# Performance work log

Measured on AMD Instinct MI355X. Metric: run time of the kernel, lower is better.

## Reference

```python
import jax, jax.numpy as jnp
import numpy as np

B, N, E, H, DEPTH = 2, 2048, 1024, 8, 12
D = E // H // 2  # head_dim = 64
LN_EPS = 1e-5


def setup_inputs() -> dict:
    key = jax.random.key(0)
    ks = jax.random.split(key, 10)
    w = lambda k: jax.random.normal(k, (E, E), jnp.float32) * (E ** -0.5)
    lp = lambda k: jax.random.normal(k, (D,), jnp.float32) * 0.1
    return {
        "x": jax.random.normal(ks[0], (B, N, E), jnp.float32),
        "Wq": w(ks[1]), "Wk": w(ks[2]), "Wv": w(ks[3]), "Wo": w(ks[4]),
        "lq1": lp(ks[5]), "lk1": lp(ks[6]), "lq2": lp(ks[7]), "lk2": lp(ks[8]),
        "ln_g": jnp.ones((2 * D,), jnp.float32),
        "ln_b": jnp.zeros((2 * D,), jnp.float32),
    }


def reference(x, Wq, Wk, Wv, Wo, lq1, lk1, lq2, lk2, ln_g, ln_b):
    b, n, e = x.shape
    lam_init = 0.8 - 0.6 * np.exp(-0.3 * DEPTH)  # lambda_init_fn(depth)
    # projections; split into 2H half-heads of dim D for q,k; H heads of dim 2D for v
    q = (x @ Wq).reshape(b, n, 2 * H, D).transpose(0, 2, 1, 3) * (D ** -0.5)  # [b,2H,n,D]
    k = (x @ Wk).reshape(b, n, 2 * H, D).transpose(0, 2, 1, 3)                # [b,2H,n,D]
    v = (x @ Wv).reshape(b, n, H, 2 * D).transpose(0, 2, 1, 3)                # [b,H,n,2D]
    scores = jnp.einsum('bhqd,bhkd->bhqk', q, k)                              # [b,2H,n,n]
    attn = jax.nn.softmax(scores, axis=-1).reshape(b, H, 2, n, n)
    lam = jnp.exp(jnp.sum(lq1 * lk1)) - jnp.exp(jnp.sum(lq2 * lk2)) + lam_init
    w_diff = attn[:, :, 0] - lam * attn[:, :, 1]                              # [b,H,n,n]
    o = jnp.einsum('bhqk,bhkd->bhqd', w_diff, v)                              # [b,H,n,2D]
    # per-head LayerNorm over channel dim 2D
    mu = o.mean(-1, keepdims=True)
    var = ((o - mu) ** 2).mean(-1, keepdims=True)
    o = (o - mu) * jax.lax.rsqrt(var + LN_EPS) * ln_g + ln_b
    o = o.transpose(0, 2, 1, 3).reshape(b, n, e)
    return o @ Wo
```

## Files before the change

kernel.cpp:

```cpp
#include <hip/hip_runtime.h>
#include <hip/hip_bf16.h>
#include <math.h>

#define B_ 2
#define N_ 2048
#define E_ 1024
#define H_ 8

typedef __attribute__((ext_vector_type(8))) short frag8;
typedef __attribute__((ext_vector_type(4))) float f32x4;
typedef __attribute__((ext_vector_type(16))) float f32x16;
typedef __attribute__((ext_vector_type(8))) unsigned short u16x8;

constexpr float LAM_INIT = 0.7836057665316245f;
constexpr float LOG2E = 1.4426950408889634f;
constexpr float EXP2_GUARD = -23.083120654f;

static __device__ __forceinline__ float fast_exp2(float x) {
#if __has_builtin(__builtin_amdgcn_exp2f)
  return __builtin_amdgcn_exp2f(x);
#else
  return exp2f(x);
#endif
}

static __device__ __forceinline__ ushort f2bf(float f) {
  union { float f; unsigned u; } v; v.f = f;
  unsigned r = (v.u + 0x7FFFu + ((v.u >> 16) & 1u)) >> 16;
  return (ushort)r;
}

static __device__ __forceinline__ unsigned pkbf(float a, float b) {
  __hip_bfloat162 h = __float22bfloat162_rn(make_float2(a, b));
  return *(unsigned*)&h;
}

static __device__ __forceinline__ float bf2f_lo(unsigned u) {
  union { unsigned u; float f; } v; v.u = u << 16; return v.f;
}
static __device__ __forceinline__ float bf2f_hi(unsigned u) {
  union { unsigned u; float f; } v; v.u = u & 0xFFFF0000u; return v.f;
}

static __device__ __forceinline__ void async16(const void* g, void* l) {
  __builtin_amdgcn_global_load_lds((const __attribute__((address_space(1))) void*)g,
                                   (__attribute__((address_space(3))) void*)l, 16, 0, 0);
}

static __device__ __forceinline__ frag8 mkfrag(unsigned p0, unsigned p1,
                                               unsigned p2, unsigned p3) {
  auto r02 = __builtin_amdgcn_permlane32_swap((int)p0, (int)p2, false, false);
  auto r13 = __builtin_amdgcn_permlane32_swap((int)p1, (int)p3, false, false);
  union { unsigned u[4]; frag8 f; } u;
  u.u[0] = (unsigned)r02[0];
  u.u[1] = (unsigned)r13[0];
  u.u[2] = (unsigned)r02[1];
  u.u[3] = (unsigned)r13[1];
  return u.f;
}

__global__ __launch_bounds__(256) void prep_kernel(
    const float* __restrict__ x,
    const float* __restrict__ Wq, const float* __restrict__ Wk,
    const float* __restrict__ Wv, const float* __restrict__ Wo,
    const float* __restrict__ lq1, const float* __restrict__ lk1,
    const float* __restrict__ lq2, const float* __restrict__ lk2,
    ushort* __restrict__ xb, ushort* __restrict__ wqkvt, ushort* __restrict__ wot,
    float* __restrict__ lam_out) {
  __shared__ ushort t[64][72];
  const int bx = blockIdx.x;
  const int tid = threadIdx.x;
  if (bx < 2048) {
    int i = bx * 256 + tid;
    const float4* sp = (const float4*)x + (size_t)i * 2;
    float4 a = sp[0], b = sp[1];
    u16x8 o;
    o[0] = f2bf(a.x); o[1] = f2bf(a.y); o[2] = f2bf(a.z); o[3] = f2bf(a.w);
    o[4] = f2bf(b.x); o[5] = f2bf(b.y); o[6] = f2bf(b.z); o[7] = f2bf(b.w);
    *(u16x8*)(xb + (size_t)i * 8) = o;
  } else if (bx < 3072) {
    int idx = bx - 2048;
    int sel = idx >> 8, rem = idx & 255;
    const float* W = (sel == 0) ? Wq : (sel == 1) ? Wk : (sel == 2) ? Wv : Wo;
    ushort* Wt = (sel < 3) ? (wqkvt + (size_t)sel * 1048576) : wot;
    const int c0 = (rem & 15) * 64, r0 = (rem >> 4) * 64;
    {
      int r = tid >> 2, cc = (tid & 3) * 16;
      const float* sp = W + (size_t)(r0 + r) * 1024 + c0 + cc;
      #pragma unroll
      for (int j = 0; j < 4; j++) {
        float4 a = *(const float4*)(sp + j * 4);
        t[cc + j * 4 + 0][r] = f2bf(a.x);
        t[cc + j * 4 + 1][r] = f2bf(a.y);
        t[cc + j * 4 + 2][r] = f2bf(a.z);
        t[cc + j * 4 + 3][r] = f2bf(a.w);
      }
    }
    __syncthreads();
    int c = tid >> 2, rr = (tid & 3) * 16;
    ushort* dp = Wt + (size_t)(c0 + c) * 1024 + r0 + rr;
    *(u16x8*)dp = *(u16x8*)&t[c][rr];
    *(u16x8*)(dp + 8) = *(u16x8*)&t[c][rr + 8];
  } else {
    if (tid < 64) {
      float t1 = lq1[tid] * lk1[tid];
      float t2 = lq2[tid] * lk2[tid];
      #pragma unroll
      for (int off = 32; off > 0; off >>= 1) {
        t1 += __shfl_down(t1, off);
        t2 += __shfl_down(t2, off);
      }
      if (tid == 0) lam_out[0] = expf(t1) - expf(t2) + LAM_INIT;
    }
  }
}

__global__ __launch_bounds__(256) void gemm_qkv(const ushort* __restrict__ xb,
                                                const ushort* __restrict__ wqkvt,
                                                ushort* __restrict__ qkb,
                                                ushort* __restrict__ vtb, float qscale) {
  __shared__ ushort As[4096];
  __shared__ ushort Bs[4096];
  const int id = blockIdx.x;
  const ushort* A; const ushort* Bt; ushort* C;
  int m0, n0, ldc;
  float sc;
  if (id < 512) {
    m0 = (id >> 4) * 128; n0 = (id & 15) * 128;
    A = xb; Bt = wqkvt; C = qkb; ldc = 2048;
    sc = (n0 < 1024) ? qscale : 1.0f;
  } else {
    int id2 = id - 512;
    m0 = (id2 & 7) * 128; n0 = (id2 >> 3) * 128;
    A = wqkvt + 2 * 1048576; Bt = xb; C = vtb; ldc = 4096;
    sc = 1.0f;
  }
  const int tid = threadIdx.x;
  const int w = tid >> 6, l = tid & 63;
  const int quad = l >> 4, col16 = l & 15;
  const int wm = (w & 1) * 64, wn = (w >> 1) * 64;
  const int lrow = l >> 2, lcol = (l & 3) * 8;

  f32x4 acc[4][4];
  #pragma unroll
  for (int mt = 0; mt < 4; mt++)
    #pragma unroll
    for (int nt = 0; nt < 4; nt++) acc[mt][nt] = (f32x4){0.f, 0.f, 0.f, 0.f};

  for (int k0 = 0; k0 < 1024; k0 += 32) {
    __syncthreads();
    #pragma unroll
    for (int i = 0; i < 4; i++) {
      int s = w * 4 + i;
      if (s < 8) {
        const ushort* gp = A + (size_t)(m0 + s * 16 + lrow) * 1024 + k0 + lcol;
        async16(gp, (char*)As + s * 1024);
      } else {
        int s2 = s - 8;
        const ushort* gp = Bt + (size_t)(n0 + s2 * 16 + lrow) * 1024 + k0 + lcol;
        async16(gp, (char*)Bs + s2 * 1024);
      }
    }
    __syncthreads();
    frag8 af[4], bfr[4];
    #pragma unroll
    for (int mt = 0; mt < 4; mt++)
      af[mt] = *(const frag8*)((const char*)As + (wm + mt * 16 + col16) * 64 + quad * 16);
    #pragma unroll
    for (int nt = 0; nt < 4; nt++)
      bfr[nt] = *(const frag8*)((const char*)Bs + (wn + nt * 16 + col16) * 64 + quad * 16);
    #pragma unroll
    for (int mt = 0; mt < 4; mt++)
      #pragma unroll
      for (int nt = 0; nt < 4; nt++)
        acc[mt][nt] = __builtin_amdgcn_mfma_f32_16x16x32_bf16(af[mt], bfr[nt], acc[mt][nt], 0, 0, 0);
  }

  #pragma unroll
  for (int mt = 0; mt < 4; mt++)
    #pragma unroll
    for (int r = 0; r < 4; r++) {
      int m = m0 + wm + mt * 16 + quad * 4 + r;
      #pragma unroll
      for (int nt = 0; nt < 4; nt++) {
        int n = n0 + wn + nt * 16 + col16;
        C[(size_t)m * ldc + n] = f2bf(acc[mt][nt][r] * sc);
      }
    }
}

__global__ __launch_bounds__(256) void gemm_out(const ushort* __restrict__ A,
                                                const ushort* __restrict__ Bt,
                                                float* __restrict__ Cp) {
  __shared__ ushort As[2048];
  __shared__ ushort Bs[4096];
  const int tid = threadIdx.x;
  const int w = tid >> 6, l = tid & 63;
  const int quad = l >> 4, col16 = l & 15;
  const int m0 = blockIdx.y * 64, n0 = blockIdx.x * 128;
  const int wm = (w & 1) * 32, wn = (w >> 1) * 64;
  const int lrow = l >> 2, lcol = (l & 3) * 8;

  f32x4 acc[2][4];
  #pragma unroll
  for (int mt = 0; mt < 2; mt++)
    #pragma unroll
    for (int nt = 0; nt < 4; nt++) acc[mt][nt] = (f32x4){0.f, 0.f, 0.f, 0.f};

  for (int k0 = 0; k0 < 1024; k0 += 32) {
    __syncthreads();
    #pragma unroll
    for (int i = 0; i < 3; i++) {
      int s = w * 3 + i;
      if (s < 4) {
        const ushort* gp = A + (size_t)(m0 + s * 16 + lrow) * 1024 + k0 + lcol;
        async16(gp, (char*)As + s * 1024);
      } else {
        int s2 = s - 4;
        const ushort* gp = Bt + (size_t)(n0 + s2 * 16 + lrow) * 1024 + k0 + lcol;
        async16(gp, (char*)Bs + s2 * 1024);
      }
    }
    __syncthreads();
    frag8 af[2], bfr[4];
    #pragma unroll
    for (int mt = 0; mt < 2; mt++)
      af[mt] = *(const frag8*)((const char*)As + (wm + mt * 16 + col16) * 64 + quad * 16);
    #pragma unroll
    for (int nt = 0; nt < 4; nt++)
      bfr[nt] = *(const frag8*)((const char*)Bs + (wn + nt * 16 + col16) * 64 + quad * 16);
    #pragma unroll
    for (int mt = 0; mt < 2; mt++)
      #pragma unroll
      for (int nt = 0; nt < 4; nt++)
        acc[mt][nt] = __builtin_amdgcn_mfma_f32_16x16x32_bf16(af[mt], bfr[nt], acc[mt][nt], 0, 0, 0);
  }

  #pragma unroll
  for (int mt = 0; mt < 2; mt++)
    #pragma unroll
    for (int r = 0; r < 4; r++) {
      int m = m0 + wm + mt * 16 + quad * 4 + r;
      #pragma unroll
      for (int nt = 0; nt < 4; nt++) {
        int n = n0 + wn + nt * 16 + col16;
        Cp[(size_t)m * 1024 + n] = acc[mt][nt][r];
      }
    }
}

__global__ __launch_bounds__(512, 2) void flash_kernel(const ushort* __restrict__ qk,
                                                       const ushort* __restrict__ vt,
                                                       const float* __restrict__ lam_p,
                                                       const float* __restrict__ ln_g,
                                                       const float* __restrict__ ln_b,
                                                       ushort* __restrict__ onorm) {
  const int L = blockIdx.x;
  const int hb = (L & 7) | (((L >> 3) & 1) << 3);
  const int qb = L >> 4;
  const int h = hb & 7, b = hb >> 3;

  const int tid = threadIdx.x;
  const int w = tid >> 6;
  const int hsel = w >> 2;
  const int h2 = 2 * h + hsel;
  const int lane31 = tid & 31, half = (tid & 63) >> 5;
  const int qloc = (w & 3) * 32 + lane31;
  const int i0 = qb * 128 + (w & 3) * 32;

  __shared__ char bufA[32768], bufB[32768];
  __shared__ float epi[128 * 128];
  __shared__ float epi_l[128];

  const float lam = lam_p[0];

  frag8 qf[4];
  #pragma unroll
  for (int chk = 0; chk < 4; chk++) {
    const ushort* qp = qk + (size_t)(b * N_ + i0 + lane31) * 2048 +
                       h2 * 64 + chk * 16 + half * 8;
    qf[chk] = *(const frag8*)qp;
  }

  f32x16 o_[4];
  #pragma unroll
  for (int cm = 0; cm < 4; cm++)
    #pragma unroll
    for (int i = 0; i < 16; i++) o_[cm][i] = 0.f;
  float la0 = 0.f, la1 = 0.f;

  auto stage = [&](int k0, char* buf) {
    {
      int row = tid >> 3, sch = (tid & 7) ^ (row & 7);
      const ushort* kg = qk + (size_t)(b * N_ + k0 + row) * 2048 + 1024 + (2 * h) * 64 + sch * 8;
      async16(kg, buf + w * 1024);
    }
    {
      int row = tid >> 3, sch = (tid & 7) ^ (row & 7);
      const ushort* kg = qk + (size_t)(b * N_ + k0 + row) * 2048 + 1024 + (2 * h + 1) * 64 + sch * 8;
      async16(kg, buf + 8192 + w * 1024);
    }
    #pragma unroll
    for (int it = 0; it < 2; it++) {
      int j = it * 512 + tid;
      int row = j >> 3, sch = (j & 7) ^ (row & 7);
      const ushort* vg = vt + (size_t)(h * 128 + row) * 4096 + b * N_ + k0 + sch * 8;
      async16(vg, buf + 16384 + it * 8192 + w * 1024);
    }
  };

  auto compute = [&](const char* buf) {
    const char* Kb = buf + hsel * 8192;
    const char* Vb = buf + 16384;
    #pragma unroll
    for (int kh = 0; kh < 2; kh++) {
      f32x16 st;
      #pragma unroll
      for (int i = 0; i < 16; i++) st[i] = EXP2_GUARD;
      const int r = kh * 32 + lane31;
      __builtin_amdgcn_s_setprio(1);
      #pragma unroll
      for (int chk = 0; chk < 4; chk++) {
        frag8 a = *(const frag8*)(Kb + r * 128 + (((chk << 1) | half) ^ (r & 7)) * 16);
        st = __builtin_amdgcn_mfma_f32_32x32x16_bf16(a, qf[chk], st, 0, 0, 0);
      }
      __builtin_amdgcn_s_setprio(0);
      unsigned pk[8];
      #pragma unroll
      for (int p = 0; p < 8; p++) {
        float e0 = fast_exp2(st[2 * p]);
        float e1 = fast_exp2(st[2 * p + 1]);
        la0 += e0;
        la1 += e1;
        pk[p] = pkbf(e0, e1);
      }
      #pragma unroll
      for (int c16 = 0; c16 < 2; c16++) {
        frag8 bfr = mkfrag(pk[c16 * 4 + 0], pk[c16 * 4 + 1],
                           pk[c16 * 4 + 2], pk[c16 * 4 + 3]);
        __builtin_amdgcn_s_setprio(1);
        #pragma unroll
        for (int cm = 0; cm < 4; cm++) {
          int c = cm * 32 + lane31;
          int g = (kh * 4 + c16 * 2 + half) ^ (c & 7);
          frag8 a = *(const frag8*)(Vb + c * 128 + g * 16);
          o_[cm] = __builtin_amdgcn_mfma_f32_32x32x16_bf16(a, bfr, o_[cm], 0, 0, 0);
        }
        __builtin_amdgcn_s_setprio(0);
      }
    }
  };

  stage(0, bufA);
  #pragma unroll 1
  for (int kt2 = 0; kt2 < 16; kt2++) {
    const int k0 = kt2 * 128;
    __syncthreads();
    stage(k0 + 64, bufB);
    compute(bufA);
    __syncthreads();
    if (kt2 < 15)
      stage(k0 + 128, bufA);
    compute(bufB);
  }

  float l_acc = la0 + la1;
  float lt = l_acc + __shfl_xor(l_acc, 32);

  if (hsel == 1) {
    if (half == 0) epi_l[qloc] = lt;
    #pragma unroll
    for (int cm = 0; cm < 4; cm++)
      #pragma unroll
      for (int g = 0; g < 4; g++) {
        int c = cm * 32 + g * 8 + half * 4;
        int pch = (c >> 2) ^ (qloc & 31);
        *(f32x4*)&epi[qloc * 128 + pch * 4] =
            (f32x4){o_[cm][4 * g + 0], o_[cm][4 * g + 1],
                    o_[cm][4 * g + 2], o_[cm][4 * g + 3]};
      }
  }
  __syncthreads();
  if (hsel == 0) {
    const float rle = 1.0f / lt;
    const float rlo = 1.0f / epi_l[qloc];
    float sum = 0.f, ss = 0.f;
    #pragma unroll
    for (int cm = 0; cm < 4; cm++)
      #pragma unroll
      for (int g = 0; g < 4; g++) {
        int c = cm * 32 + g * 8 + half * 4;
        int pch = (c >> 2) ^ (qloc & 31);
        f32x4 ov = *(const f32x4*)&epi[qloc * 128 + pch * 4];
        #pragma unroll
        for (int j = 0; j < 4; j++) {
          float v = o_[cm][4 * g + j] * rle - lam * ov[j] * rlo;
          o_[cm][4 * g + j] = v;
          sum += v;
          ss += v * v;
        }
      }
    sum += __shfl_xor(sum, 32);
    ss += __shfl_xor(ss, 32);
    float mu = sum * (1.0f / 128.0f);
    float var = ss * (1.0f / 128.0f) - mu * mu;
    float rr = rsqrtf(var + 1e-5f);
    int q = qb * 128 + qloc;
    ushort* ob = onorm + ((size_t)(b * N_ + q)) * E_ + h * 128;
    #pragma unroll
    for (int cm = 0; cm < 4; cm++)
      #pragma unroll
      for (int g = 0; g < 4; g++) {
        int c = cm * 32 + g * 8 + half * 4;
        float4 g4 = *(const float4*)&ln_g[c];
        float4 b4 = *(const float4*)&ln_b[c];
        float v0 = (o_[cm][4 * g + 0] - mu) * rr * g4.x + b4.x;
        float v1 = (o_[cm][4 * g + 1] - mu) * rr * g4.y + b4.y;
        float v2 = (o_[cm][4 * g + 2] - mu) * rr * g4.z + b4.z;
        float v3 = (o_[cm][4 * g + 3] - mu) * rr * g4.w + b4.w;
        uint2 pv;
        pv.x = pkbf(v0, v1);
        pv.y = pkbf(v2, v3);
        *(uint2*)(ob + c) = pv;
      }
  }
}

extern "C" void kernel_launch(void* const* d_in, const int* in_sizes, int n_in,
                              void* d_out, int out_size, void* d_ws, size_t ws_size,
                              hipStream_t stream) {
  const float* x    = (const float*)d_in[0];
  const float* Wq   = (const float*)d_in[1];
  const float* Wk   = (const float*)d_in[2];
  const float* Wv   = (const float*)d_in[3];
  const float* Wo   = (const float*)d_in[4];
  const float* lq1  = (const float*)d_in[5];
  const float* lk1  = (const float*)d_in[6];
  const float* lq2  = (const float*)d_in[7];
  const float* lk2  = (const float*)d_in[8];
  const float* ln_g = (const float*)d_in[9];
  const float* ln_b = (const float*)d_in[10];
  float* out = (float*)d_out;

  const size_t MN = (size_t)B_ * N_ * E_;
  ushort* xb    = (ushort*)d_ws;
  ushort* wqkvt = xb + MN;
  ushort* wot   = wqkvt + 3 * 1048576;
  ushort* qkb   = wot + 1048576;
  ushort* vtb   = qkb + (size_t)4096 * 2048;
  float*  lam   = (float*)(vtb + MN);
  ushort* onorm = xb;

  prep_kernel<<<dim3(3073), 256, 0, stream>>>(x, Wq, Wk, Wv, Wo, lq1, lk1, lq2, lk2,
                                              xb, wqkvt, wot, lam);

  gemm_qkv<<<dim3(768), 256, 0, stream>>>(xb, wqkvt, qkb, vtb, 0.125f * LOG2E);

  flash_kernel<<<dim3(256), 512, 0, stream>>>(qkb, vtb, lam, ln_g, ln_b, onorm);

  gemm_out<<<dim3(8, 64), 256, 0, stream>>>(onorm, wot, out);
}
```

Measured before the change: 211.4 us.

## Store V in MFMA-fragment layout and load it directly from global memory

The QKV GEMM now writes V transposed into a blocked layout matching the 32x32x16 MFMA A-fragment, so the attention kernel loads V fragments straight from global/L2 into registers instead of staging them through LDS. This shrinks LDS staging to K only and aliases the epilogue buffer onto the staging buffers, lowering LDS use per block. The cost is that V loads become synchronous register loads that are no longer overlapped by async LDS copies, with added register pressure and a new barrier before the epilogue reuse.

```diff
diff --git a/kernel.cpp b/kernel.cpp
--- a/kernel.cpp
+++ b/kernel.cpp
@@ -33,13 +33,6 @@
 static __device__ __forceinline__ unsigned pkbf(float a, float b) {
   __hip_bfloat162 h = __float22bfloat162_rn(make_float2(a, b));
   return *(unsigned*)&h;
-}
-
-static __device__ __forceinline__ float bf2f_lo(unsigned u) {
-  union { unsigned u; float f; } v; v.u = u << 16; return v.f;
-}
-static __device__ __forceinline__ float bf2f_hi(unsigned u) {
-  union { unsigned u; float f; } v; v.u = u & 0xFFFF0000u; return v.f;
 }
 
 static __device__ __forceinline__ void async16(const void* g, void* l) {
@@ -123,16 +116,16 @@
   __shared__ ushort Bs[4096];
   const int id = blockIdx.x;
   const ushort* A; const ushort* Bt; ushort* C;
-  int m0, n0, ldc;
+  int m0, n0;
   float sc;
   if (id < 512) {
     m0 = (id >> 4) * 128; n0 = (id & 15) * 128;
-    A = xb; Bt = wqkvt; C = qkb; ldc = 2048;
+    A = xb; Bt = wqkvt; C = qkb;
     sc = (n0 < 1024) ? qscale : 1.0f;
   } else {
     int id2 = id - 512;
     m0 = (id2 & 7) * 128; n0 = (id2 >> 3) * 128;
-    A = wqkvt + 2 * 1048576; Bt = xb; C = vtb; ldc = 4096;
+    A = wqkvt + 2 * 1048576; Bt = xb; C = vtb;
     sc = 1.0f;
   }
   const int tid = threadIdx.x;
@@ -176,17 +169,35 @@
         acc[mt][nt] = __builtin_amdgcn_mfma_f32_16x16x32_bf16(af[mt], bfr[nt], acc[mt][nt], 0, 0, 0);
   }
 
-  #pragma unroll
-  for (int mt = 0; mt < 4; mt++)
-    #pragma unroll
-    for (int r = 0; r < 4; r++) {
-      int m = m0 + wm + mt * 16 + quad * 4 + r;
-      #pragma unroll
-      for (int nt = 0; nt < 4; nt++) {
-        int n = n0 + wn + nt * 16 + col16;
-        C[(size_t)m * ldc + n] = f2bf(acc[mt][nt][r] * sc);
-      }
-    }
+  if (id < 512) {
+    #pragma unroll
+    for (int mt = 0; mt < 4; mt++)
+      #pragma unroll
+      for (int r = 0; r < 4; r++) {
+        int m = m0 + wm + mt * 16 + quad * 4 + r;
+        #pragma unroll
+        for (int nt = 0; nt < 4; nt++) {
+          int n = n0 + wn + nt * 16 + col16;
+          C[(size_t)m * 2048 + n] = f2bf(acc[mt][nt][r] * sc);
+        }
+      }
+  } else {
+    #pragma unroll
+    for (int mt = 0; mt < 4; mt++)
+      #pragma unroll
+      for (int r = 0; r < 4; r++) {
+        int m = m0 + wm + mt * 16 + quad * 4 + r;
+        int hh = m >> 7, c = m & 127;
+        #pragma unroll
+        for (int nt = 0; nt < 4; nt++) {
+          int n = n0 + wn + nt * 16 + col16;
+          int bb = n >> 11, k = n & 2047;
+          size_t addr = (size_t)(hh * 2 + bb) * 262144 +
+                        (size_t)((k >> 4) * 2048 + c * 16 + ((k >> 3) & 1) * 8 + (k & 7));
+          C[addr] = f2bf(acc[mt][nt][r]);
+        }
+      }
+  }
 }
 
 __global__ __launch_bounds__(256) void gemm_out(const ushort* __restrict__ A,
@@ -268,11 +279,14 @@
   const int qloc = (w & 3) * 32 + lane31;
   const int i0 = qb * 128 + (w & 3) * 32;
 
-  __shared__ char bufA[32768], bufB[32768];
-  __shared__ float epi[128 * 128];
-  __shared__ float epi_l[128];
+  __shared__ char smem[66048];
+  char* bufA = smem;
+  char* bufB = smem + 16384;
+  float* epi = (float*)smem;
+  float* epi_l = (float*)(smem + 65536);
 
   const float lam = lam_p[0];
+  const ushort* vbase = vt + (size_t)(h * 2 + b) * 262144 + (size_t)lane31 * 16 + half * 8;
 
   frag8 qf[4];
   #pragma unroll
@@ -290,30 +304,25 @@
   float la0 = 0.f, la1 = 0.f;
 
   auto stage = [&](int k0, char* buf) {
-    {
-      int row = tid >> 3, sch = (tid & 7) ^ (row & 7);
-      const ushort* kg = qk + (size_t)(b * N_ + k0 + row) * 2048 + 1024 + (2 * h) * 64 + sch * 8;
-      async16(kg, buf + w * 1024);
-    }
-    {
-      int row = tid >> 3, sch = (tid & 7) ^ (row & 7);
-      const ushort* kg = qk + (size_t)(b * N_ + k0 + row) * 2048 + 1024 + (2 * h + 1) * 64 + sch * 8;
-      async16(kg, buf + 8192 + w * 1024);
-    }
-    #pragma unroll
-    for (int it = 0; it < 2; it++) {
-      int j = it * 512 + tid;
-      int row = j >> 3, sch = (j & 7) ^ (row & 7);
-      const ushort* vg = vt + (size_t)(h * 128 + row) * 4096 + b * N_ + k0 + sch * 8;
-      async16(vg, buf + 16384 + it * 8192 + w * 1024);
-    }
+    int row = tid >> 3, sch = (tid & 7) ^ (row & 7);
+    const ushort* kg = qk + (size_t)(b * N_ + k0 + row) * 2048 + 1024 + (2 * h) * 64 + sch * 8;
+    async16(kg, buf + w * 1024);
+    async16(kg + 64, buf + 8192 + w * 1024);
   };
 
-  auto compute = [&](const char* buf) {
+  auto compute = [&](const char* buf, int t) {
     const char* Kb = buf + hsel * 8192;
-    const char* Vb = buf + 16384;
     #pragma unroll
     for (int kh = 0; kh < 2; kh++) {
+      frag8 vf[2][4];
+      {
+        const ushort* vt_t = vbase + (size_t)(t * 4 + kh * 2) * 2048;
+        #pragma unroll
+        for (int c16 = 0; c16 < 2; c16++)
+          #pragma unroll
+          for (int cm = 0; cm < 4; cm++)
+            vf[c16][cm] = *(const frag8*)(vt_t + c16 * 2048 + cm * 512);
+      }
       f32x16 st;
       #pragma unroll
       for (int i = 0; i < 16; i++) st[i] = EXP2_GUARD;
@@ -340,12 +349,8 @@
                            pk[c16 * 4 + 2], pk[c16 * 4 + 3]);
         __builtin_amdgcn_s_setprio(1);
         #pragma unroll
-        for (int cm = 0; cm < 4; cm++) {
-          int c = cm * 32 + lane31;
-          int g = (kh * 4 + c16 * 2 + half) ^ (c & 7);
-          frag8 a = *(const frag8*)(Vb + c * 128 + g * 16);
-          o_[cm] = __builtin_amdgcn_mfma_f32_32x32x16_bf16(a, bfr, o_[cm], 0, 0, 0);
-        }
+        for (int cm = 0; cm < 4; cm++)
+          o_[cm] = __builtin_amdgcn_mfma_f32_32x32x16_bf16(vf[c16][cm], bfr, o_[cm], 0, 0, 0);
         __builtin_amdgcn_s_setprio(0);
       }
     }
@@ -357,12 +362,13 @@
     const int k0 = kt2 * 128;
     __syncthreads();
     stage(k0 + 64, bufB);
-    compute(bufA);
+    compute(bufA, 2 * kt2);
     __syncthreads();
     if (kt2 < 15)
       stage(k0 + 128, bufA);
-    compute(bufB);
-  }
+    compute(bufB, 2 * kt2 + 1);
+  }
+  __syncthreads();
 
   float l_acc = la0 + la1;
   float lt = l_acc + __shfl_xor(l_acc, 32);
```

Result: slower. 233.2 us (+10.3%).
